# Optimization experiments

Hardware: AMD Instinct MI355X
Metric: run time of the kernel (lower is better)

## Reference

```python
import jax, jax.numpy as jnp
import numpy as np

N_CLASSES = 512


def setup_inputs() -> dict:
    key = jax.random.key(0)
    k1, k2 = jax.random.split(key)
    x0 = jax.random.normal(k1, (16, 8192, 1, 128), dtype=jnp.float32)
    # nn.Parameter(torch.randn(n_channels, n_classes, vec_len) * 0.001)
    embedding0 = jax.random.normal(k2, (1, N_CLASSES, 128), dtype=jnp.float32) * 0.001
    return {"x0": x0, "embedding0": embedding0}


def reference(x0, embedding0):
    # normalize=False path: x = x0, embedding = embedding0
    x = x0
    embedding = embedding0
    B, S, C, L = x.shape
    K = embedding.shape[1]
    xf = x.reshape(B * S, C, L)

    x2 = jnp.sum(xf * xf, axis=-1)                      # (BS, C)
    e2 = jnp.sum(embedding * embedding, axis=-1)        # (C, K)
    dot = jnp.einsum('bcl,ckl->bck', xf, embedding)     # (BS, C, K)
    d2 = x2[:, :, None] - 2.0 * dot + e2[None]          # (BS, C, K)
    index = jnp.argmin(d2, axis=2)                      # (BS, C)

    # entropy of code usage histogram (divided by BS, as in the torch code)
    hist = jnp.zeros((K,), dtype=jnp.float32).at[index.reshape(-1)].add(1.0)
    prob = hist / jnp.float32(index.shape[0])
    entropy = -jnp.sum(jnp.where(prob > 0, prob * jnp.log(jnp.where(prob > 0, prob, 1.0)), 0.0))

    # gather selected codebook vectors: (BS, C, L) -> (B, S, C, L)
    output = embedding[jnp.arange(C)[None, :], index].reshape(B, S, C, L)

    sg = jax.lax.stop_gradient
    out0 = sg(output - x) + x                                   # straight-through
    out1 = jnp.sum((sg(x) - output) ** 2, axis=-1)              # (B, S, C)
    out2 = jnp.sum((x - sg(output)) ** 2, axis=-1) + jnp.sum((x - x0) ** 2, axis=-1)
    return out0, out1, out2, entropy
```

## Files before the change

### kernel.cpp

```cpp
#include <hip/hip_runtime.h>
#include <hip/hip_bf16.h>
#include <math.h>

#define NROWS 131072
#define NCODE 512
#define DIM 128
#define ESCALE 256.0f
#define DESCALE 0.0078125f

typedef long long llong;
typedef __attribute__((ext_vector_type(16))) float f32x16;

__device__ inline llong mk_ll(int lo, int hi) {
    return ((llong)(unsigned long long)(unsigned)hi << 32) | (unsigned)lo;
}

__device__ inline float kstuff(float sv, int code) {
    return __uint_as_float((__float_as_uint(sv) & 0xFFFFFE00u) | (unsigned)code);
}

__global__ __launch_bounds__(256) void prep_pack8(const float* __restrict__ emb,
        int4* __restrict__ afp, float* __restrict__ e2p) {
    __shared__ float part[32][8];
    const int tid = threadIdx.x;
    const int mt = blockIdx.x;
    const int lane = tid & 63, q = tid >> 6;
    const int c5 = lane & 31, g = lane >> 5;
    const int code = mt * 32 + c5;
    const float* src = emb + (size_t)code * DIM;

    int w[4];
    float ss = 0.f;
    #pragma unroll
    for (int h = 0; h < 2; ++h) {
        int d0 = (2 * q + h) * 16 + g * 8;
        float4 v0 = *reinterpret_cast<const float4*>(src + d0);
        float4 v1 = *reinterpret_cast<const float4*>(src + d0 + 4);
        ss = fmaf(v0.x, v0.x, ss); ss = fmaf(v0.y, v0.y, ss);
        ss = fmaf(v0.z, v0.z, ss); ss = fmaf(v0.w, v0.w, ss);
        ss = fmaf(v1.x, v1.x, ss); ss = fmaf(v1.y, v1.y, ss);
        ss = fmaf(v1.z, v1.z, ss); ss = fmaf(v1.w, v1.w, ss);
        int lo = __builtin_amdgcn_cvt_pk_fp8_f32(v0.x * ESCALE, v0.y * ESCALE, 0, false);
        lo = __builtin_amdgcn_cvt_pk_fp8_f32(v0.z * ESCALE, v0.w * ESCALE, lo, true);
        int hi = __builtin_amdgcn_cvt_pk_fp8_f32(v1.x * ESCALE, v1.y * ESCALE, 0, false);
        hi = __builtin_amdgcn_cvt_pk_fp8_f32(v1.z * ESCALE, v1.w * ESCALE, hi, true);
        w[2 * h] = lo; w[2 * h + 1] = hi;
    }
    afp[(mt * 4 + q) * 64 + lane] = make_int4(w[0], w[1], w[2], w[3]);
    part[c5][q * 2 + g] = ss;
    __syncthreads();
    if (tid < 32) {
        float s = 0.f;
        #pragma unroll
        for (int j = 0; j < 8; ++j) s += part[tid][j];
        int g2 = (tid >> 2) & 1;
        int r = (tid & 3) | ((tid >> 3) << 2);
        e2p[mt * 32 + g2 * 16 + r] = s;
    }
}

__global__ __launch_bounds__(256, 4) void vq_argmin(
        const float* __restrict__ x, const float* __restrict__ emb,
        const int4* __restrict__ afp, const float* __restrict__ e2p,
        int* __restrict__ idxg,
        float* __restrict__ out0, float* __restrict__ out1, float* __restrict__ out2) {
    __shared__ unsigned char xs8[128][DIM];
    __shared__ float x2s[128];
    __shared__ float s_m[2][2][64];
    __shared__ int   s_fidx[2][64];

    const int tid = threadIdx.x;
    const int lane = tid & 63, l31 = lane & 31, g = lane >> 5;
    const long row0 = (long)blockIdx.x * 128;

    {
        const float4* xg = reinterpret_cast<const float4*>(x + row0 * DIM);
        #pragma unroll
        for (int it = 0; it < 16; ++it) {
            float4 v = xg[it * 256 + tid];
            int r = it * 8 + (tid >> 5), c = tid & 31;
            float s = v.x * v.x + v.y * v.y + v.z * v.z + v.w * v.w;
            s += __shfl_xor(s, 1);  s += __shfl_xor(s, 2);
            s += __shfl_xor(s, 4);  s += __shfl_xor(s, 8);
            s += __shfl_xor(s, 16);
            if ((tid & 31) == 0) x2s[r] = s;
            int w = __builtin_amdgcn_cvt_pk_fp8_f32(v.x, v.y, 0, false);
            w = __builtin_amdgcn_cvt_pk_fp8_f32(v.z, v.w, w, true);
            int off = (c * 4) ^ ((r & 15) << 3);
            *reinterpret_cast<int*>(&xs8[r][off]) = w;
        }
    }
    __syncthreads();

    const int wv = tid >> 6, rg = wv >> 1, ch = wv & 1;
    const int r0 = rg * 64 + l31;
    const int r1 = rg * 64 + 32 + l31;

    #define RB(RR, K) *reinterpret_cast<const llong*>(&xs8[RR][((K) * 16 + g * 8) ^ (((RR) & 15) << 3)])
    const llong b0 = RB(r0, 0), b1 = RB(r0, 1), b2 = RB(r0, 2), b3 = RB(r0, 3);
    const llong b4 = RB(r0, 4), b5 = RB(r0, 5), b6 = RB(r0, 6), b7 = RB(r0, 7);
    const llong c0 = RB(r1, 0), c1 = RB(r1, 1), c2 = RB(r1, 2), c3 = RB(r1, 3);
    const llong c4 = RB(r1, 4), c5 = RB(r1, 5), c6 = RB(r1, 6), c7 = RB(r1, 7);
    #undef RB

    float m1a = 1e30f, m1b = 1e30f;

    #pragma unroll 1
    for (int t = 0; t < 8; ++t) {
        const int mt = ch * 8 + t;
        const int4* ap = afp + mt * 256 + lane;
        int4 A0 = ap[0];
        int4 A1 = ap[64];
        int4 A2 = ap[128];
        int4 A3 = ap[192];
        f32x16 acc0 = {}, acc1 = {};
        acc0 = __builtin_amdgcn_mfma_f32_32x32x16_fp8_fp8(mk_ll(A0.x, A0.y), b0, acc0, 0, 0, 0);
        acc1 = __builtin_amdgcn_mfma_f32_32x32x16_fp8_fp8(mk_ll(A0.x, A0.y), c0, acc1, 0, 0, 0);
        acc0 = __builtin_amdgcn_mfma_f32_32x32x16_fp8_fp8(mk_ll(A0.z, A0.w), b1, acc0, 0, 0, 0);
        acc1 = __builtin_amdgcn_mfma_f32_32x32x16_fp8_fp8(mk_ll(A0.z, A0.w), c1, acc1, 0, 0, 0);
        acc0 = __builtin_amdgcn_mfma_f32_32x32x16_fp8_fp8(mk_ll(A1.x, A1.y), b2, acc0, 0, 0, 0);
        acc1 = __builtin_amdgcn_mfma_f32_32x32x16_fp8_fp8(mk_ll(A1.x, A1.y), c2, acc1, 0, 0, 0);
        acc0 = __builtin_amdgcn_mfma_f32_32x32x16_fp8_fp8(mk_ll(A1.z, A1.w), b3, acc0, 0, 0, 0);
        acc1 = __builtin_amdgcn_mfma_f32_32x32x16_fp8_fp8(mk_ll(A1.z, A1.w), c3, acc1, 0, 0, 0);
        acc0 = __builtin_amdgcn_mfma_f32_32x32x16_fp8_fp8(mk_ll(A2.x, A2.y), b4, acc0, 0, 0, 0);
        acc1 = __builtin_amdgcn_mfma_f32_32x32x16_fp8_fp8(mk_ll(A2.x, A2.y), c4, acc1, 0, 0, 0);
        acc0 = __builtin_amdgcn_mfma_f32_32x32x16_fp8_fp8(mk_ll(A2.z, A2.w), b5, acc0, 0, 0, 0);
        acc1 = __builtin_amdgcn_mfma_f32_32x32x16_fp8_fp8(mk_ll(A2.z, A2.w), c5, acc1, 0, 0, 0);
        acc0 = __builtin_amdgcn_mfma_f32_32x32x16_fp8_fp8(mk_ll(A3.x, A3.y), b6, acc0, 0, 0, 0);
        acc1 = __builtin_amdgcn_mfma_f32_32x32x16_fp8_fp8(mk_ll(A3.x, A3.y), c6, acc1, 0, 0, 0);
        acc0 = __builtin_amdgcn_mfma_f32_32x32x16_fp8_fp8(mk_ll(A3.z, A3.w), b7, acc0, 0, 0, 0);
        acc1 = __builtin_amdgcn_mfma_f32_32x32x16_fp8_fp8(mk_ll(A3.z, A3.w), c7, acc1, 0, 0, 0);

        const float4* ev = reinterpret_cast<const float4*>(e2p + mt * 32 + g * 16);
        const int base = mt * 32 + 4 * g;
        float4 ea = ev[0], eb = ev[1], ec = ev[2], ed = ev[3];
        float earr[16] = {ea.x, ea.y, ea.z, ea.w, eb.x, eb.y, eb.z, eb.w,
                          ec.x, ec.y, ec.z, ec.w, ed.x, ed.y, ed.z, ed.w};
        float k0[16], k1[16];
        #pragma unroll
        for (int r = 0; r < 16; ++r) {
            int code = base + (r & 3) + 8 * (r >> 2);
            k0[r] = kstuff(earr[r] - DESCALE * acc0[r], code);
            k1[r] = kstuff(earr[r] - DESCALE * acc1[r], code);
        }
        #pragma unroll
        for (int s = 8; s > 0; s >>= 1)
            #pragma unroll
            for (int r = 0; r < s; ++r) {
                k0[r] = fminf(k0[r], k0[r + s]);
                k1[r] = fminf(k1[r], k1[r + s]);
            }
        m1a = fminf(m1a, k0[0]);
        m1b = fminf(m1b, k1[0]);
    }

    m1a = fminf(m1a, __shfl_xor(m1a, 32));
    m1b = fminf(m1b, __shfl_xor(m1b, 32));
    if (lane < 32) {
        s_m[rg][ch][l31] = m1a;
        s_m[rg][ch][32 + l31] = m1b;
    }
    __syncthreads();

    if (tid < 128) {
        int rgx = tid >> 6, lr = tid & 63;
        float m1f = fminf(s_m[rgx][0][lr], s_m[rgx][1][lr]);
        unsigned kb = __float_as_uint(m1f);
        int i1f = (int)(kb & 0x1FFu);
        float sv = __uint_as_float(kb & 0xFFFFFE00u);
        long row = row0 + tid;
        idxg[row] = i1f;
        s_fidx[rgx][lr] = i1f;
        float o = x2s[tid] + sv;
        out1[row] = o;
        out2[row] = o;
    }
    __syncthreads();

    {
        const float4* e4 = reinterpret_cast<const float4*>(emb);
        float4* o4 = reinterpret_cast<float4*>(out0);
        const int rb = wv * 32;
        #pragma unroll 4
        for (int rx = 0; rx < 32; rx += 2) {
            int lr = rb + rx + g;
            int c = s_fidx[lr >> 6][lr & 63];
            o4[(row0 + lr) * 32 + l31] = e4[c * 32 + l31];
        }
    }
}

__global__ __launch_bounds__(256) void hist_part(const int* __restrict__ idxg,
        int* __restrict__ partial) {
    __shared__ int h[NCODE];
    const int tid = threadIdx.x, b = blockIdx.x;
    h[tid] = 0; h[tid + 256] = 0;
    __syncthreads();
    const int4* i4 = reinterpret_cast<const int4*>(idxg + b * 2048);
    #pragma unroll
    for (int k = 0; k < 2; ++k) {
        int4 v = i4[k * 256 + tid];
        atomicAdd(&h[v.x], 1); atomicAdd(&h[v.y], 1);
        atomicAdd(&h[v.z], 1); atomicAdd(&h[v.w], 1);
    }
    __syncthreads();
    partial[b * NCODE + tid] = h[tid];
    partial[b * NCODE + 256 + tid] = h[tid + 256];
}

__global__ void entropy_kernel(const int* __restrict__ partial,
        float* __restrict__ oent) {
    __shared__ float red[8];
    int tid = threadIdx.x;
    int c = 0;
    #pragma unroll
    for (int b = 0; b < 64; ++b) c += partial[b * NCODE + tid];
    float p = (float)c * (1.0f / 131072.0f);
    float t = (p > 0.f) ? (-p * logf(p)) : 0.f;
    #pragma unroll
    for (int off = 32; off > 0; off >>= 1) t += __shfl_down(t, off);
    if ((tid & 63) == 0) red[tid >> 6] = t;
    __syncthreads();
    if (tid == 0) {
        float s = 0.f;
        #pragma unroll
        for (int i = 0; i < 8; ++i) s += red[i];
        *oent = s;
    }
}

extern "C" void kernel_launch(void* const* d_in, const int* in_sizes, int n_in,
                              void* d_out, int out_size, void* d_ws, size_t ws_size,
                              hipStream_t stream) {
    const float* x   = (const float*)d_in[0];
    const float* emb = (const float*)d_in[1];
    float* out  = (float*)d_out;
    float* out0 = out;
    float* out1 = out0 + (size_t)NROWS * DIM;
    float* out2 = out1 + NROWS;
    float* oent = out2 + NROWS;

    float* e2p = (float*)d_ws;
    int4*  afp = (int4*)((char*)d_ws + 4096);
    int*   idxg = (int*)((char*)d_ws + 4096 + 65536);
    int*   partial = (int*)((char*)d_ws + 4096 + 65536 + 524288);

    prep_pack8<<<16, 256, 0, stream>>>(emb, afp, e2p);
    vq_argmin<<<NROWS / 128, 256, 0, stream>>>(x, emb, afp, e2p, idxg, out0, out1, out2);
    hist_part<<<64, 256, 0, stream>>>(idxg, partial);
    entropy_kernel<<<1, NCODE, 0, stream>>>(partial, oent);
}
```

Before: 47.28 us.

## Give each wave the full codebook and drop cross-wave argmin reduction

```diff
diff --git a/kernel.cpp b/kernel.cpp
--- a/kernel.cpp
+++ b/kernel.cpp
@@ -59,15 +59,13 @@
     }
 }
 
-__global__ __launch_bounds__(256, 4) void vq_argmin(
+__global__ __launch_bounds__(128, 4) void vq_argmin(
         const float* __restrict__ x, const float* __restrict__ emb,
         const int4* __restrict__ afp, const float* __restrict__ e2p,
         int* __restrict__ idxg,
         float* __restrict__ out0, float* __restrict__ out1, float* __restrict__ out2) {
     __shared__ unsigned char xs8[128][DIM];
     __shared__ float x2s[128];
-    __shared__ float s_m[2][2][64];
-    __shared__ int   s_fidx[2][64];
 
     const int tid = threadIdx.x;
     const int lane = tid & 63, l31 = lane & 31, g = lane >> 5;
@@ -76,9 +74,10 @@
     {
         const float4* xg = reinterpret_cast<const float4*>(x + row0 * DIM);
         #pragma unroll
-        for (int it = 0; it < 16; ++it) {
-            float4 v = xg[it * 256 + tid];
-            int r = it * 8 + (tid >> 5), c = tid & 31;
+        for (int it = 0; it < 32; ++it) {
+            int i = it * 128 + tid;
+            float4 v = xg[i];
+            int r = i >> 5, c = i & 31;
             float s = v.x * v.x + v.y * v.y + v.z * v.z + v.w * v.w;
             s += __shfl_xor(s, 1);  s += __shfl_xor(s, 2);
             s += __shfl_xor(s, 4);  s += __shfl_xor(s, 8);
@@ -92,9 +91,9 @@
     }
     __syncthreads();
 
-    const int wv = tid >> 6, rg = wv >> 1, ch = wv & 1;
-    const int r0 = rg * 64 + l31;
-    const int r1 = rg * 64 + 32 + l31;
+    const int wv = tid >> 6;
+    const int r0 = wv * 64 + l31;
+    const int r1 = wv * 64 + 32 + l31;
 
     #define RB(RR, K) *reinterpret_cast<const llong*>(&xs8[RR][((K) * 16 + g * 8) ^ (((RR) & 15) << 3)])
     const llong b0 = RB(r0, 0), b1 = RB(r0, 1), b2 = RB(r0, 2), b3 = RB(r0, 3);
@@ -106,8 +105,7 @@
     float m1a = 1e30f, m1b = 1e30f;
 
     #pragma unroll 1
-    for (int t = 0; t < 8; ++t) {
-        const int mt = ch * 8 + t;
+    for (int mt = 0; mt < 16; ++mt) {
         const int4* ap = afp + mt * 256 + lane;
         int4 A0 = ap[0];
         int4 A1 = ap[64];
@@ -156,36 +154,38 @@
 
     m1a = fminf(m1a, __shfl_xor(m1a, 32));
     m1b = fminf(m1b, __shfl_xor(m1b, 32));
+    const unsigned ka = __float_as_uint(m1a), kbb = __float_as_uint(m1b);
+    const int idxa = (int)(ka & 0x1FFu), idxb = (int)(kbb & 0x1FFu);
+    const float sva = __uint_as_float(ka & 0xFFFFFE00u);
+    const float svb = __uint_as_float(kbb & 0xFFFFFE00u);
+
     if (lane < 32) {
-        s_m[rg][ch][l31] = m1a;
-        s_m[rg][ch][32 + l31] = m1b;
-    }
-    __syncthreads();
-
-    if (tid < 128) {
-        int rgx = tid >> 6, lr = tid & 63;
-        float m1f = fminf(s_m[rgx][0][lr], s_m[rgx][1][lr]);
-        unsigned kb = __float_as_uint(m1f);
-        int i1f = (int)(kb & 0x1FFu);
-        float sv = __uint_as_float(kb & 0xFFFFFE00u);
-        long row = row0 + tid;
-        idxg[row] = i1f;
-        s_fidx[rgx][lr] = i1f;
-        float o = x2s[tid] + sv;
-        out1[row] = o;
-        out2[row] = o;
-    }
-    __syncthreads();
+        long rowA = row0 + r0;
+        long rowB = row0 + r1;
+        idxg[rowA] = idxa;
+        idxg[rowB] = idxb;
+        float oa = x2s[r0] + sva;
+        float ob = x2s[r1] + svb;
+        out1[rowA] = oa; out2[rowA] = oa;
+        out1[rowB] = ob; out2[rowB] = ob;
+    }
 
     {
         const float4* e4 = reinterpret_cast<const float4*>(emb);
-        float4* o4 = reinterpret_cast<float4*>(out0);
-        const int rb = wv * 32;
+        float4* o4 = reinterpret_cast<float4*>(out0) + (row0 + wv * 64) * 32;
         #pragma unroll 4
         for (int rx = 0; rx < 32; rx += 2) {
-            int lr = rb + rx + g;
-            int c = s_fidx[lr >> 6][lr & 63];
-            o4[(row0 + lr) * 32 + l31] = e4[c * 32 + l31];
+            int ca = __shfl(idxa, rx);
+            int cb = __shfl(idxa, rx + 1);
+            int c = g ? cb : ca;
+            o4[(rx + g) * 32 + l31] = e4[c * 32 + l31];
+        }
+        #pragma unroll 4
+        for (int rx = 0; rx < 32; rx += 2) {
+            int ca = __shfl(idxb, rx);
+            int cb = __shfl(idxb, rx + 1);
+            int c = g ? cb : ca;
+            o4[(32 + rx + g) * 32 + l31] = e4[c * 32 + l31];
         }
     }
 }
@@ -246,7 +246,7 @@
     int*   partial = (int*)((char*)d_ws + 4096 + 65536 + 524288);
 
     prep_pack8<<<16, 256, 0, stream>>>(emb, afp, e2p);
-    vq_argmin<<<NROWS / 128, 256, 0, stream>>>(x, emb, afp, e2p, idxg, out0, out1, out2);
+    vq_argmin<<<NROWS / 128, 128, 0, stream>>>(x, emb, afp, e2p, idxg, out0, out1, out2);
     hist_part<<<64, 256, 0, stream>>>(idxg, partial);
     entropy_kernel<<<1, NCODE, 0, stream>>>(partial, oent);
 }
```

After: 62.08 us. 1.31x slower.
